# Kernel tuning notes

Measured on AMD Instinct MI355X. Metric: run time of the kernel, lower is better.

Reference implementation:

```python
import jax, jax.numpy as jnp
import numpy as np

E, L, M, F, S, P = 4, 10, 512, 128, 1000, 10  # envs, labels, max_sample, features, sample_size, batch_len


def setup_inputs() -> dict:
    key = jax.random.key(0)
    k1, k2, k3 = jax.random.split(key, 3)
    data_len = jax.random.randint(k1, (E, L), M // 2, M + 1, dtype=jnp.int32)
    matrix = jax.random.normal(k2, (E, L, M, F), dtype=jnp.float32)
    # zero out padded samples beyond data_len (as shape_to_matrix does)
    pad_mask = jnp.arange(M)[None, None, :, None] < data_len[:, :, None, None]
    matrix = matrix * pad_mask
    params = jnp.eye(F, dtype=jnp.float32) + 0.01 * jax.random.normal(k3, (F, F), dtype=jnp.float32)
    is_train_env = jnp.array([True, True, False, False])
    return {"matrix": matrix, "params": params, "data_len": data_len, "is_train_env": is_train_env}


def reference(matrix, params, data_len, is_train_env):
    lenf = data_len.astype(matrix.dtype)  # [E,L], torch keeps this as float32
    # __init__ preprocessing: normalize by mean std over sample dim (detached in torch)
    std = jax.lax.stop_gradient(jnp.std(matrix, axis=2).mean())
    mat = matrix / std
    # Silverman-style bandwidth on the normalized matrix (detached in torch)
    bw = jax.lax.stop_gradient(1.06 * (M ** (-1.0 / 5.0)) * jnp.std(mat, axis=2).mean())
    offset = jnp.exp(-0.5 / bw ** 2)
    proj = jnp.einsum('elmf,fg->elmg', mat, params)  # [E,L,M,F]
    left = jax.lax.stop_gradient(proj.min())   # .item() in torch -> constant
    right = jax.lax.stop_gradient(proj.max())
    delta = (right - left) / S
    x_grid = jnp.linspace(left, right, S)
    divisor = jnp.sqrt(2.0 * jnp.pi) * bw

    def step(acc, points):  # points: [P] grid chunk
        d2 = (proj[..., None] - points) ** 2                     # [E,L,M,F,P]
        s = jnp.sum(offset ** d2, axis=2)                        # [E,L,F,P]
        # remove contribution of zero-padded samples, then normalize by true count
        corr = (M - lenf)[:, :, None] * (offset ** (points ** 2))[None, None, :]  # [E,L,P]
        r = (s - corr[:, :, None, :]) / lenf[:, :, None, None]   # [E,L,F,P]
        d = jnp.sum(jnp.abs(r[:, None] - r[None, :]), axis=-1)   # [E,E,L,F] pairwise L1 over grid chunk
        return acc + d, None

    store_dis, _ = jax.lax.scan(step, jnp.zeros((E, E, L, F), proj.dtype), x_grid.reshape(S // P, P))
    store_dis = store_dis / divisor  # [E,E,L,F]

    idx = jnp.arange(E)
    upper = idx[:, None] < idx[None, :]                                   # all env pairs i<j
    train_pair = upper & is_train_env[:, None] & is_train_env[None, :]    # train env pairs i<j
    half = store_dis * (delta / 2.0)
    neg = jnp.array(-jnp.inf, half.dtype)
    test_results = jnp.where(upper[:, :, None, None], half, neg).max(axis=(0, 1))        # [L,F]
    train_results = jnp.where(train_pair[:, :, None, None], half, neg).max(axis=(0, 1))  # [L,F]
    train_dis = train_results.max(axis=0).mean()
    test_dis = test_results.max(axis=0).mean()
    return train_results, test_results, train_dis, test_dis
```

## Files before the change

### kernel.cpp

```cpp
#include <hip/hip_runtime.h>
#include <cmath>

#define E_ 4
#define L_ 10
#define M_ 512
#define F_ 128
#define S_ 1000

typedef unsigned int u32;
typedef _Float16 f16;
typedef __attribute__((ext_vector_type(8))) _Float16 v8h;
typedef __attribute__((ext_vector_type(4))) float v4f;

__device__ __forceinline__ float fexp2(float a){
#if __has_builtin(__builtin_amdgcn_exp2f)
  return __builtin_amdgcn_exp2f(a);
#else
  return exp2f(a);
#endif
}


__global__ __launch_bounds__(256) void k_pre(const float* __restrict__ mat,
                       const float* __restrict__ par,
                       float* __restrict__ projT, float* __restrict__ wsf){
  __shared__ float sm[2048];
  int b = blockIdx.x, tid = threadIdx.x;
  if (b >= 1280){
    int el = b - 1280;
    int fq = (tid & 31) * 4, part = tid >> 5;
    const float* base = mat + ((size_t)el * M_ + part*64) * F_;
    float4 s  = make_float4(0.f,0.f,0.f,0.f);
    float4 s2 = make_float4(0.f,0.f,0.f,0.f);
    #pragma unroll 8
    for (int i = 0; i < 64; i++){
      float4 v = *(const float4*)&base[i*F_ + fq];
      s.x += v.x; s.y += v.y; s.z += v.z; s.w += v.w;
      s2.x += v.x*v.x; s2.y += v.y*v.y; s2.z += v.z*v.z; s2.w += v.w*v.w;
    }
    ((float4*)sm)[tid]       = s;
    ((float4*)sm)[256 + tid] = s2;
    __syncthreads();
    for (int g = 4; g >= 1; g >>= 1){
      if (part < g){
        float4 o  = ((float4*)sm)[tid + g*32];
        float4 o2 = ((float4*)sm)[256 + tid + g*32];
        s.x += o.x; s.y += o.y; s.z += o.z; s.w += o.w;
        s2.x += o2.x; s2.y += o2.y; s2.z += o2.z; s2.w += o2.w;
        ((float4*)sm)[tid] = s;
        ((float4*)sm)[256 + tid] = s2;
      }
      __syncthreads();
    }
    if (part == 0){
      *(float4*)&wsf[2576 + el*128 + fq] = s;
      *(float4*)&wsf[7696 + el*128 + fq] = s2;
    }
    return;
  }
  int el = b >> 5, mt = (b & 31) * 16;
  int lane = tid & 63, wave = tid >> 6;
  int q = (lane >> 4) & 3, m16 = lane & 15;
  const float* arow = mat + ((size_t)el * M_ + mt + m16) * F_;
  v4f acc0 = {0.f,0.f,0.f,0.f}, acc1 = {0.f,0.f,0.f,0.f};
  #pragma unroll
  for (int c = 0; c < 4; c++){
    float4 a0 = *(const float4*)&arow[c*32 + q*8];
    float4 a1 = *(const float4*)&arow[c*32 + q*8 + 4];
    v8h af, b0, b1;
    af[0]=(f16)a0.x; af[1]=(f16)a0.y; af[2]=(f16)a0.z; af[3]=(f16)a0.w;
    af[4]=(f16)a1.x; af[5]=(f16)a1.y; af[6]=(f16)a1.z; af[7]=(f16)a1.w;
    const float* pb = par + (c*32 + q*8)*F_ + wave*32 + m16;
    #pragma unroll
    for (int j = 0; j < 8; j++){
      b0[j] = (f16)pb[j*F_];
      b1[j] = (f16)pb[j*F_ + 16];
    }
    acc0 = __builtin_amdgcn_mfma_f32_16x16x32_f16(af, b0, acc0, 0, 0, 0);
    acc1 = __builtin_amdgcn_mfma_f32_16x16x32_f16(af, b1, acc1, 0, 0, 0);
  }
  *(float4*)(projT + ((size_t)el*F_ + wave*32      + m16)*M_ + mt + q*4)
      = make_float4(acc0[0], acc0[1], acc0[2], acc0[3]);
  *(float4*)(projT + ((size_t)el*F_ + wave*32 + 16 + m16)*M_ + mt + q*4)
      = make_float4(acc1[0], acc1[1], acc1[2], acc1[3]);
  float lmin =  3.4e38f, lmax = -3.4e38f;
  #pragma unroll
  for (int r = 0; r < 4; r++){
    lmin = fminf(lmin, fminf(acc0[r], acc1[r]));
    lmax = fmaxf(lmax, fmaxf(acc0[r], acc1[r]));
  }
  #pragma unroll
  for (int d = 32; d >= 1; d >>= 1){
    lmin = fminf(lmin, __shfl_xor(lmin, d, 64));
    lmax = fmaxf(lmax, __shfl_xor(lmax, d, 64));
  }
  if (lane == 0){ sm[wave] = lmin; sm[8+wave] = lmax; }
  __syncthreads();
  if (tid == 0){
    wsf[16   + b] = fminf(fminf(sm[0], sm[1]), fminf(sm[2], sm[3]));
    wsf[1296 + b] = fmaxf(fmaxf(sm[8], sm[9]), fmaxf(sm[10], sm[11]));
  }
}

__global__ __launch_bounds__(1024) void k_red(float* __restrict__ wsf,
                                              float divisor, float k2c){
  __shared__ float rmn[1024], rmx[1024], rs[1024];
  int tid = threadIdx.x;
  float mn = 3.4e38f, mx = -3.4e38f, s = 0.f;
  for (int i = tid; i < 1280; i += 1024){
    mn = fminf(mn, wsf[16   + i]);
    mx = fmaxf(mx, wsf[1296 + i]);
  }
  for (int i = tid; i < 5120; i += 1024){
    float a  = wsf[2576 + i];
    float a2 = wsf[7696 + i];
    float mean = a * (1.0f/512.0f);
    float var  = a2 * (1.0f/512.0f) - mean*mean;
    s += sqrtf(fmaxf(var, 0.0f));
  }
  rmn[tid] = mn; rmx[tid] = mx; rs[tid] = s;
  __syncthreads();
  for (int g = 512; g >= 1; g >>= 1){
    if (tid < g){
      rmn[tid] = fminf(rmn[tid], rmn[tid+g]);
      rmx[tid] = fmaxf(rmx[tid], rmx[tid+g]);
      rs[tid] += rs[tid+g];
    }
    __syncthreads();
  }
  float rstd   = 5120.0f / rs[0];
  float leftS  = rmn[0] * rstd;
  float rightS = rmx[0] * rstd;
  float stepFS = (rightS - leftS) * (1.0f/999.0f);
  if (tid == 0){
    float inv2 = 1.0f / (2.0f * stepFS);
    wsf[0] = rstd * inv2;
    wsf[1] = leftS * inv2;
    wsf[2] = stepFS;
    wsf[3] = leftS;
    wsf[8] = ((rightS - leftS) * (1.0f/1000.0f)) * 0.5f / divisor;
  }
  float sh = 2.0f * stepFS;
  if (tid < 152){
    float v = 0.f;
    if (tid >= 8){
      int pr = (tid >> 1) - 4;
      int u  = pr - 34;
      float d = (tid & 1) ? (float)(2*u-1) * sh : (float)(2*u) * sh;
      v = (pr < 69) ? fexp2(k2c*d*d) : 0.f;
    }
    wsf[16 + tid] = v;
  }
  if (tid >= 256 && tid < 512){
    int idx = tid - 256;
    float xc = fmaf((float)(idx - 1), 4.0f*stepFS, leftS);
    wsf[168 + idx] = fexp2(k2c * xc * xc);
  }
}

__global__ __launch_bounds__(256) void k_kde(const float* __restrict__ projT,
                      const int* __restrict__ dlen, const float* __restrict__ wsf,
                      float* __restrict__ dpair){
  __shared__ __align__(16) float smem[4752];
  int b = blockIdx.x;
  int l = b >> 7, f = b & 127;
  int tid = threadIdx.x, wave = tid >> 6, lane = tid & 63;
  int e = wave;
  const float4* gp = (const float4*)(projT + (((size_t)e * L_ + l) * F_ + f) * M_);
  float4 g0 = gp[lane], g1 = gp[lane + 64];
  float posScale = wsf[0], posOff = wsf[1];
  for (int idx = tid; idx < 824; idx += 256)
    ((float4*)(smem + 1024))[idx] = make_float4(0.f,0.f,0.f,0.f);
  if (tid < 38)
    ((float4*)(smem + 4320))[tid] = ((const float4*)(wsf + 16))[tid];
  if (tid >= 64 && tid < 128)
    ((float4*)(smem + 4472))[tid - 64] = ((const float4*)(wsf + 168))[tid - 64];
  __syncthreads();
  {
    float* hf = smem + 1024 + e*824;
    float pv[8] = {g0.x,g0.y,g0.z,g0.w,g1.x,g1.y,g1.z,g1.w};
    #pragma unroll
    for (int i = 0; i < 8; i++){
      float pos = fmaf(pv[i], posScale, -posOff);
      float n = floorf(pos + 0.5f);
      float d = pos - n;
      float wm = 0.5f*(0.5f-d)*(0.5f-d);
      float wp = 0.5f*(0.5f+d)*(0.5f+d);
      float w0 = 0.75f - d*d;
      int b0 = (int)n + 71;
      int b1 = b0 + 1, b2 = b0 + 2;
      int W0 = b0 + ((b0>>3)<<1);
      int W1 = b1 + ((b1>>3)<<1);
      int W2 = b2 + ((b2>>3)<<1);
      atomicAdd(&hf[W0], wm);
      atomicAdd(&hf[W1], w0);
      atomicAdd(&hf[W2], wp);
    }
  }
  __syncthreads();
  float lenE = (float)dlen[e*L_ + l];
  float rlen = 1.0f / lenE;
  float padc = 512.0f - lenE;
  {
    const float2* sK2 = (const float2*)(smem + 4320);
    const float* hl = smem + 1024 + e*824 + 10*lane;
    float2 c0 = sK2[72], c1 = sK2[73], c2 = sK2[74], c3 = sK2[75];
    float a0=0.f, a1=0.f, a2=0.f, a3=0.f;
    #pragma unroll
    for (int i = 1; i <= 72; i++){
      float2 H = *(const float2*)&hl[2*i + 2*(i>>2)];
      a0 = fmaf(H.x, c0.x, fmaf(H.y, c0.y, a0));
      a1 = fmaf(H.x, c1.x, fmaf(H.y, c1.y, a1));
      a2 = fmaf(H.x, c2.x, fmaf(H.y, c2.y, a2));
      a3 = fmaf(H.x, c3.x, fmaf(H.y, c3.y, a3));
      c3 = c2; c2 = c1; c1 = c0; c0 = sK2[72 - i];
    }
    int o0 = 4*lane;
    float4 cr = *(const float4*)&smem[4472 + o0];
    float4 stv = make_float4((a0 - padc*cr.x)*rlen, (a1 - padc*cr.y)*rlen,
                             (a2 - padc*cr.z)*rlen, (a3 - padc*cr.w)*rlen);
    *(float4*)&smem[e*256 + o0] = stv;
  }
  __syncthreads();
  float ps[6] = {0,0,0,0,0,0};
  if (tid < 250){
    float x[4][4];
    #pragma unroll
    for (int ee=0; ee<4; ee++){
      const float* st = &smem[ee*256 + tid];
      x[ee][0]=st[0]; x[ee][1]=st[1]; x[ee][2]=st[2]; x[ee][3]=st[3];
    }
    #pragma unroll
    for (int k=0; k<4; k++){
      float u = (float)k * 0.25f;
      float um1 = u - 1.0f, um2 = u - 2.0f, up1 = u + 1.0f;
      float w0 = -u * um1 * um2 * (1.0f/6.0f);
      float w1 = up1 * um1 * um2 * 0.5f;
      float w2 = -u * up1 * um2 * 0.5f;
      float w3 = u * up1 * um1 * (1.0f/6.0f);
      float rr[4];
      #pragma unroll
      for (int ee=0; ee<4; ee++)
        rr[ee] = w0*x[ee][0] + w1*x[ee][1] + w2*x[ee][2] + w3*x[ee][3];
      ps[0] += fabsf(rr[0]-rr[1]);
      ps[1] += fabsf(rr[0]-rr[2]);
      ps[2] += fabsf(rr[0]-rr[3]);
      ps[3] += fabsf(rr[1]-rr[2]);
      ps[4] += fabsf(rr[1]-rr[3]);
      ps[5] += fabsf(rr[2]-rr[3]);
    }
  }
  #pragma unroll
  for (int pr=0; pr<6; pr++){
    float v = ps[pr];
    #pragma unroll
    for (int d=32; d>=1; d>>=1) v += __shfl_xor(v, d, 64);
    if (lane == 0) smem[4728 + wave*6 + pr] = v;
  }
  __syncthreads();
  if (tid < 6)
    dpair[tid*1280 + b] = smem[4728+tid] + smem[4734+tid] + smem[4740+tid] + smem[4746+tid];
}

__global__ void k_fin(const float* __restrict__ dpair, const float* __restrict__ wsf,
                      const int* __restrict__ istrain, float* __restrict__ out){
  __shared__ float str[1280], ste[1280];
  __shared__ float s1[128], s2[128];
  int tid = threadIdx.x;
  float hscale = wsf[8];
  bool t0 = istrain[0]!=0, t1 = istrain[1]!=0, t2 = istrain[2]!=0, t3 = istrain[3]!=0;
  bool trn[6] = { t0&&t1, t0&&t2, t0&&t3, t1&&t2, t1&&t3, t2&&t3 };
  for (int idx = tid; idx < 1280; idx += 256){
    float tmax = -INFINITY, trmax = -INFINITY;
    #pragma unroll
    for (int pr=0;pr<6;pr++){
      float h = dpair[pr*1280 + idx] * hscale;
      tmax = fmaxf(tmax, h);
      if (trn[pr]) trmax = fmaxf(trmax, h);
    }
    out[idx]        = trmax;
    out[1280 + idx] = tmax;
    str[idx] = trmax; ste[idx] = tmax;
  }
  __syncthreads();
  if (tid < 128){
    float m1 = -INFINITY, m2 = -INFINITY;
    for (int l=0;l<L_;l++){
      m1 = fmaxf(m1, str[l*F_ + tid]);
      m2 = fmaxf(m2, ste[l*F_ + tid]);
    }
    s1[tid] = m1; s2[tid] = m2;
  }
  __syncthreads();
  for (int g=64; g>=1; g>>=1){
    if (tid < g){ s1[tid] += s1[tid+g]; s2[tid] += s2[tid+g]; }
    __syncthreads();
  }
  if (tid == 0){
    out[2560] = s1[0] * (1.0f/128.0f);
    out[2561] = s2[0] * (1.0f/128.0f);
  }
}

extern "C" void kernel_launch(void* const* d_in, const int* in_sizes, int n_in,
                              void* d_out, int out_size, void* d_ws, size_t ws_size,
                              hipStream_t stream){
  const float* mat = (const float*)d_in[0];
  const float* par = (const float*)d_in[1];
  const int*  dlen = (const int*)d_in[2];
  const int*  istr = (const int*)d_in[3];
  float* out   = (float*)d_out;
  float* wsf   = (float*)d_ws;
  float* dpair = wsf + 12816;
  float* projT = wsf + 20496;

  double bw_d   = 1.06 * pow(512.0, -0.2);
  float  bw     = (float)bw_d;
  float  offset = expf(-0.5f / (bw*bw));
  float  k2c    = (float)(log((double)offset) * 1.4426950408889634);
  float  divisor = sqrtf(6.283185307179586f) * bw;

  k_pre <<<1320, 256, 0, stream>>>(mat, par, projT, wsf);
  k_red <<<1,   1024, 0, stream>>>(wsf, divisor, k2c);
  k_kde <<<1280, 256, 0, stream>>>(projT, dlen, wsf, dpair);
  k_fin <<<1,    256, 0, stream>>>(dpair, wsf, istr, out);
}
```

Measured before the change: 142.2 us.

## Fuse single-block reduction kernels into producers via last-block atomic counters

The separate one-block reduction kernel and the final reduction kernel are removed. Each producer kernel now bumps a global atomic counter after a threadfence, and the last block to finish runs the reduction. This cuts two kernel launches and their launch gaps, at the cost of a memset to reset the counters, extra fences in every block, and a serial tail done by a single 256-thread block. The dlen load is also hoisted ahead of the histogram phase.

```diff
diff --git a/kernel.cpp b/kernel.cpp
--- a/kernel.cpp
+++ b/kernel.cpp
@@ -23,8 +23,10 @@
 
 __global__ __launch_bounds__(256) void k_pre(const float* __restrict__ mat,
                        const float* __restrict__ par,
-                       float* __restrict__ projT, float* __restrict__ wsf){
+                       float* __restrict__ projT, float* __restrict__ wsf,
+                       int* __restrict__ ctr, float divisor, float k2c){
   __shared__ float sm[2048];
+  __shared__ int lastFlag;
   int b = blockIdx.x, tid = threadIdx.x;
   if (b >= 1280){
     int el = b - 1280;
@@ -56,112 +58,115 @@
       *(float4*)&wsf[2576 + el*128 + fq] = s;
       *(float4*)&wsf[7696 + el*128 + fq] = s2;
     }
-    return;
-  }
-  int el = b >> 5, mt = (b & 31) * 16;
-  int lane = tid & 63, wave = tid >> 6;
-  int q = (lane >> 4) & 3, m16 = lane & 15;
-  const float* arow = mat + ((size_t)el * M_ + mt + m16) * F_;
-  v4f acc0 = {0.f,0.f,0.f,0.f}, acc1 = {0.f,0.f,0.f,0.f};
-  #pragma unroll
-  for (int c = 0; c < 4; c++){
-    float4 a0 = *(const float4*)&arow[c*32 + q*8];
-    float4 a1 = *(const float4*)&arow[c*32 + q*8 + 4];
-    v8h af, b0, b1;
-    af[0]=(f16)a0.x; af[1]=(f16)a0.y; af[2]=(f16)a0.z; af[3]=(f16)a0.w;
-    af[4]=(f16)a1.x; af[5]=(f16)a1.y; af[6]=(f16)a1.z; af[7]=(f16)a1.w;
-    const float* pb = par + (c*32 + q*8)*F_ + wave*32 + m16;
-    #pragma unroll
-    for (int j = 0; j < 8; j++){
-      b0[j] = (f16)pb[j*F_];
-      b1[j] = (f16)pb[j*F_ + 16];
-    }
-    acc0 = __builtin_amdgcn_mfma_f32_16x16x32_f16(af, b0, acc0, 0, 0, 0);
-    acc1 = __builtin_amdgcn_mfma_f32_16x16x32_f16(af, b1, acc1, 0, 0, 0);
-  }
-  *(float4*)(projT + ((size_t)el*F_ + wave*32      + m16)*M_ + mt + q*4)
-      = make_float4(acc0[0], acc0[1], acc0[2], acc0[3]);
-  *(float4*)(projT + ((size_t)el*F_ + wave*32 + 16 + m16)*M_ + mt + q*4)
-      = make_float4(acc1[0], acc1[1], acc1[2], acc1[3]);
-  float lmin =  3.4e38f, lmax = -3.4e38f;
-  #pragma unroll
-  for (int r = 0; r < 4; r++){
-    lmin = fminf(lmin, fminf(acc0[r], acc1[r]));
-    lmax = fmaxf(lmax, fmaxf(acc0[r], acc1[r]));
-  }
-  #pragma unroll
-  for (int d = 32; d >= 1; d >>= 1){
-    lmin = fminf(lmin, __shfl_xor(lmin, d, 64));
-    lmax = fmaxf(lmax, __shfl_xor(lmax, d, 64));
-  }
-  if (lane == 0){ sm[wave] = lmin; sm[8+wave] = lmax; }
-  __syncthreads();
-  if (tid == 0){
-    wsf[16   + b] = fminf(fminf(sm[0], sm[1]), fminf(sm[2], sm[3]));
-    wsf[1296 + b] = fmaxf(fmaxf(sm[8], sm[9]), fmaxf(sm[10], sm[11]));
-  }
-}
-
-__global__ __launch_bounds__(1024) void k_red(float* __restrict__ wsf,
-                                              float divisor, float k2c){
-  __shared__ float rmn[1024], rmx[1024], rs[1024];
-  int tid = threadIdx.x;
-  float mn = 3.4e38f, mx = -3.4e38f, s = 0.f;
-  for (int i = tid; i < 1280; i += 1024){
-    mn = fminf(mn, wsf[16   + i]);
-    mx = fmaxf(mx, wsf[1296 + i]);
-  }
-  for (int i = tid; i < 5120; i += 1024){
-    float a  = wsf[2576 + i];
-    float a2 = wsf[7696 + i];
-    float mean = a * (1.0f/512.0f);
-    float var  = a2 * (1.0f/512.0f) - mean*mean;
-    s += sqrtf(fmaxf(var, 0.0f));
-  }
-  rmn[tid] = mn; rmx[tid] = mx; rs[tid] = s;
-  __syncthreads();
-  for (int g = 512; g >= 1; g >>= 1){
-    if (tid < g){
-      rmn[tid] = fminf(rmn[tid], rmn[tid+g]);
-      rmx[tid] = fmaxf(rmx[tid], rmx[tid+g]);
-      rs[tid] += rs[tid+g];
-    }
-    __syncthreads();
-  }
-  float rstd   = 5120.0f / rs[0];
-  float leftS  = rmn[0] * rstd;
-  float rightS = rmx[0] * rstd;
-  float stepFS = (rightS - leftS) * (1.0f/999.0f);
-  if (tid == 0){
-    float inv2 = 1.0f / (2.0f * stepFS);
-    wsf[0] = rstd * inv2;
-    wsf[1] = leftS * inv2;
-    wsf[2] = stepFS;
-    wsf[3] = leftS;
-    wsf[8] = ((rightS - leftS) * (1.0f/1000.0f)) * 0.5f / divisor;
-  }
-  float sh = 2.0f * stepFS;
-  if (tid < 152){
-    float v = 0.f;
-    if (tid >= 8){
-      int pr = (tid >> 1) - 4;
-      int u  = pr - 34;
-      float d = (tid & 1) ? (float)(2*u-1) * sh : (float)(2*u) * sh;
-      v = (pr < 69) ? fexp2(k2c*d*d) : 0.f;
-    }
-    wsf[16 + tid] = v;
-  }
-  if (tid >= 256 && tid < 512){
-    int idx = tid - 256;
-    float xc = fmaf((float)(idx - 1), 4.0f*stepFS, leftS);
-    wsf[168 + idx] = fexp2(k2c * xc * xc);
+  } else {
+    int el = b >> 5, mt = (b & 31) * 16;
+    int lane = tid & 63, wave = tid >> 6;
+    int q = (lane >> 4) & 3, m16 = lane & 15;
+    const float* arow = mat + ((size_t)el * M_ + mt + m16) * F_;
+    v4f acc0 = {0.f,0.f,0.f,0.f}, acc1 = {0.f,0.f,0.f,0.f};
+    #pragma unroll
+    for (int c = 0; c < 4; c++){
+      float4 a0 = *(const float4*)&arow[c*32 + q*8];
+      float4 a1 = *(const float4*)&arow[c*32 + q*8 + 4];
+      v8h af, b0, b1;
+      af[0]=(f16)a0.x; af[1]=(f16)a0.y; af[2]=(f16)a0.z; af[3]=(f16)a0.w;
+      af[4]=(f16)a1.x; af[5]=(f16)a1.y; af[6]=(f16)a1.z; af[7]=(f16)a1.w;
+      const float* pb = par + (c*32 + q*8)*F_ + wave*32 + m16;
+      #pragma unroll
+      for (int j = 0; j < 8; j++){
+        b0[j] = (f16)pb[j*F_];
+        b1[j] = (f16)pb[j*F_ + 16];
+      }
+      acc0 = __builtin_amdgcn_mfma_f32_16x16x32_f16(af, b0, acc0, 0, 0, 0);
+      acc1 = __builtin_amdgcn_mfma_f32_16x16x32_f16(af, b1, acc1, 0, 0, 0);
+    }
+    *(float4*)(projT + ((size_t)el*F_ + wave*32      + m16)*M_ + mt + q*4)
+        = make_float4(acc0[0], acc0[1], acc0[2], acc0[3]);
+    *(float4*)(projT + ((size_t)el*F_ + wave*32 + 16 + m16)*M_ + mt + q*4)
+        = make_float4(acc1[0], acc1[1], acc1[2], acc1[3]);
+    float lmin =  3.4e38f, lmax = -3.4e38f;
+    #pragma unroll
+    for (int r = 0; r < 4; r++){
+      lmin = fminf(lmin, fminf(acc0[r], acc1[r]));
+      lmax = fmaxf(lmax, fmaxf(acc0[r], acc1[r]));
+    }
+    #pragma unroll
+    for (int d = 32; d >= 1; d >>= 1){
+      lmin = fminf(lmin, __shfl_xor(lmin, d, 64));
+      lmax = fmaxf(lmax, __shfl_xor(lmax, d, 64));
+    }
+    if (lane == 0){ sm[wave] = lmin; sm[8+wave] = lmax; }
+    __syncthreads();
+    if (tid == 0){
+      wsf[16   + b] = fminf(fminf(sm[0], sm[1]), fminf(sm[2], sm[3]));
+      wsf[1296 + b] = fmaxf(fmaxf(sm[8], sm[9]), fmaxf(sm[10], sm[11]));
+    }
+  }
+  __threadfence();
+  __syncthreads();
+  if (tid == 0) lastFlag = (atomicAdd(ctr, 1) == 1319);
+  __syncthreads();
+  if (!lastFlag) return;
+  __threadfence();
+  {
+    float mn = 3.4e38f, mx = -3.4e38f, s = 0.f;
+    for (int i = tid; i < 1280; i += 256){
+      mn = fminf(mn, wsf[16   + i]);
+      mx = fmaxf(mx, wsf[1296 + i]);
+    }
+    for (int i = tid; i < 5120; i += 256){
+      float a  = wsf[2576 + i];
+      float a2 = wsf[7696 + i];
+      float mean = a * (1.0f/512.0f);
+      float var  = a2 * (1.0f/512.0f) - mean*mean;
+      s += sqrtf(fmaxf(var, 0.0f));
+    }
+    sm[tid] = mn; sm[256+tid] = mx; sm[512+tid] = s;
+    __syncthreads();
+    for (int g = 128; g >= 1; g >>= 1){
+      if (tid < g){
+        sm[tid]     = fminf(sm[tid], sm[tid+g]);
+        sm[256+tid] = fmaxf(sm[256+tid], sm[256+tid+g]);
+        sm[512+tid] += sm[512+tid+g];
+      }
+      __syncthreads();
+    }
+    float rstd   = 5120.0f / sm[512];
+    float leftS  = sm[0] * rstd;
+    float rightS = sm[256] * rstd;
+    float stepFS = (rightS - leftS) * (1.0f/999.0f);
+    if (tid == 0){
+      float inv2 = 1.0f / (2.0f * stepFS);
+      wsf[0] = rstd * inv2;
+      wsf[1] = leftS * inv2;
+      wsf[2] = stepFS;
+      wsf[3] = leftS;
+      wsf[8] = ((rightS - leftS) * (1.0f/1000.0f)) * 0.5f / divisor;
+    }
+    float sh = 2.0f * stepFS;
+    if (tid < 152){
+      float v = 0.f;
+      if (tid >= 8){
+        int pr = (tid >> 1) - 4;
+        int u  = pr - 34;
+        float d = (tid & 1) ? (float)(2*u-1) * sh : (float)(2*u) * sh;
+        v = (pr < 69) ? fexp2(k2c*d*d) : 0.f;
+      }
+      wsf[16 + tid] = v;
+    }
+    {
+      float xc = fmaf((float)(tid - 1), 4.0f*stepFS, leftS);
+      wsf[168 + tid] = fexp2(k2c * xc * xc);
+    }
   }
 }
 
 __global__ __launch_bounds__(256) void k_kde(const float* __restrict__ projT,
                       const int* __restrict__ dlen, const float* __restrict__ wsf,
-                      float* __restrict__ dpair){
+                      float* __restrict__ dpair, int* __restrict__ ctr,
+                      const int* __restrict__ istrain, float* __restrict__ out){
   __shared__ __align__(16) float smem[4752];
+  __shared__ int lastFlag;
   int b = blockIdx.x;
   int l = b >> 7, f = b & 127;
   int tid = threadIdx.x, wave = tid >> 6, lane = tid & 63;
@@ -169,6 +174,7 @@
   const float4* gp = (const float4*)(projT + (((size_t)e * L_ + l) * F_ + f) * M_);
   float4 g0 = gp[lane], g1 = gp[lane + 64];
   float posScale = wsf[0], posOff = wsf[1];
+  float lenE = (float)dlen[e*L_ + l];
   for (int idx = tid; idx < 824; idx += 256)
     ((float4*)(smem + 1024))[idx] = make_float4(0.f,0.f,0.f,0.f);
   if (tid < 38)
@@ -192,13 +198,13 @@
       int W0 = b0 + ((b0>>3)<<1);
       int W1 = b1 + ((b1>>3)<<1);
       int W2 = b2 + ((b2>>3)<<1);
-      atomicAdd(&hf[W0], wm);
-      atomicAdd(&hf[W1], w0);
-      atomicAdd(&hf[W2], wp);
-    }
-  }
-  __syncthreads();
-  float lenE = (float)dlen[e*L_ + l];
+      atomicAdd(&smem[1024 + e*824 + W0], wm);
+      atomicAdd(&smem[1024 + e*824 + W1], w0);
+      atomicAdd(&smem[1024 + e*824 + W2], wp);
+      (void)hf;
+    }
+  }
+  __syncthreads();
   float rlen = 1.0f / lenE;
   float padc = 512.0f - lenE;
   {
@@ -260,45 +266,51 @@
   __syncthreads();
   if (tid < 6)
     dpair[tid*1280 + b] = smem[4728+tid] + smem[4734+tid] + smem[4740+tid] + smem[4746+tid];
-}
-
-__global__ void k_fin(const float* __restrict__ dpair, const float* __restrict__ wsf,
-                      const int* __restrict__ istrain, float* __restrict__ out){
-  __shared__ float str[1280], ste[1280];
-  __shared__ float s1[128], s2[128];
-  int tid = threadIdx.x;
-  float hscale = wsf[8];
-  bool t0 = istrain[0]!=0, t1 = istrain[1]!=0, t2 = istrain[2]!=0, t3 = istrain[3]!=0;
-  bool trn[6] = { t0&&t1, t0&&t2, t0&&t3, t1&&t2, t1&&t3, t2&&t3 };
-  for (int idx = tid; idx < 1280; idx += 256){
-    float tmax = -INFINITY, trmax = -INFINITY;
-    #pragma unroll
-    for (int pr=0;pr<6;pr++){
-      float h = dpair[pr*1280 + idx] * hscale;
-      tmax = fmaxf(tmax, h);
-      if (trn[pr]) trmax = fmaxf(trmax, h);
-    }
-    out[idx]        = trmax;
-    out[1280 + idx] = tmax;
-    str[idx] = trmax; ste[idx] = tmax;
-  }
-  __syncthreads();
-  if (tid < 128){
-    float m1 = -INFINITY, m2 = -INFINITY;
-    for (int l=0;l<L_;l++){
-      m1 = fmaxf(m1, str[l*F_ + tid]);
-      m2 = fmaxf(m2, ste[l*F_ + tid]);
-    }
-    s1[tid] = m1; s2[tid] = m2;
-  }
-  __syncthreads();
-  for (int g=64; g>=1; g>>=1){
-    if (tid < g){ s1[tid] += s1[tid+g]; s2[tid] += s2[tid+g]; }
-    __syncthreads();
-  }
-  if (tid == 0){
-    out[2560] = s1[0] * (1.0f/128.0f);
-    out[2561] = s2[0] * (1.0f/128.0f);
+  __threadfence();
+  __syncthreads();
+  if (tid == 0) lastFlag = (atomicAdd(ctr, 1) == 1279);
+  __syncthreads();
+  if (!lastFlag) return;
+  __threadfence();
+  {
+    float* str = smem;
+    float* ste = smem + 1280;
+    float* s1  = smem + 2560;
+    float* s2  = smem + 2688;
+    float hscale = wsf[8];
+    bool t0 = istrain[0]!=0, t1 = istrain[1]!=0, t2 = istrain[2]!=0, t3 = istrain[3]!=0;
+    bool trn[6] = { t0&&t1, t0&&t2, t0&&t3, t1&&t2, t1&&t3, t2&&t3 };
+    __syncthreads();
+    for (int idx = tid; idx < 1280; idx += 256){
+      float tmax = -INFINITY, trmax = -INFINITY;
+      #pragma unroll
+      for (int pr=0;pr<6;pr++){
+        float h = dpair[pr*1280 + idx] * hscale;
+        tmax = fmaxf(tmax, h);
+        if (trn[pr]) trmax = fmaxf(trmax, h);
+      }
+      out[idx]        = trmax;
+      out[1280 + idx] = tmax;
+      str[idx] = trmax; ste[idx] = tmax;
+    }
+    __syncthreads();
+    if (tid < 128){
+      float m1 = -INFINITY, m2 = -INFINITY;
+      for (int ll=0; ll<L_; ll++){
+        m1 = fmaxf(m1, str[ll*F_ + tid]);
+        m2 = fmaxf(m2, ste[ll*F_ + tid]);
+      }
+      s1[tid] = m1; s2[tid] = m2;
+    }
+    __syncthreads();
+    for (int g=64; g>=1; g>>=1){
+      if (tid < g){ s1[tid] += s1[tid+g]; s2[tid] += s2[tid+g]; }
+      __syncthreads();
+    }
+    if (tid == 0){
+      out[2560] = s1[0] * (1.0f/128.0f);
+      out[2561] = s2[0] * (1.0f/128.0f);
+    }
   }
 }
 
@@ -313,6 +325,8 @@
   float* wsf   = (float*)d_ws;
   float* dpair = wsf + 12816;
   float* projT = wsf + 20496;
+  int*   ctr1  = (int*)(wsf + 12);
+  int*   ctr2  = (int*)(wsf + 13);
 
   double bw_d   = 1.06 * pow(512.0, -0.2);
   float  bw     = (float)bw_d;
@@ -320,8 +334,7 @@
   float  k2c    = (float)(log((double)offset) * 1.4426950408889634);
   float  divisor = sqrtf(6.283185307179586f) * bw;
 
-  k_pre <<<1320, 256, 0, stream>>>(mat, par, projT, wsf);
-  k_red <<<1,   1024, 0, stream>>>(wsf, divisor, k2c);
-  k_kde <<<1280, 256, 0, stream>>>(projT, dlen, wsf, dpair);
-  k_fin <<<1,    256, 0, stream>>>(dpair, wsf, istr, out);
+  hipMemsetAsync(wsf + 12, 0, 8, stream);
+  k_pre <<<1320, 256, 0, stream>>>(mat, par, projT, wsf, ctr1, divisor, k2c);
+  k_kde <<<1280, 256, 0, stream>>>(projT, dlen, wsf, dpair, ctr2, istr, out);
 }
```

Result: slower. 360.6 us (+153.7%).
